# Kernel tuning notes

Measured on AMD Instinct MI355X. Metric: run time of the kernel, lower is better.

Reference implementation:

```python
import jax, jax.numpy as jnp
import numpy as np


def setup_inputs() -> dict:
    key = jax.random.key(0)
    ks = jax.random.split(key, 6)
    B, C, W, H = 8, 512, 64, 64
    return {
        "x": jax.random.normal(ks[0], (B, C, W, H), dtype=jnp.float32),
        "proj_query": jax.random.normal(ks[1], (C, W, H), dtype=jnp.float32),
        "key_w": jax.random.normal(ks[2], (C, C), dtype=jnp.float32) * 0.02,
        "key_b": jax.random.normal(ks[3], (C,), dtype=jnp.float32) * 0.02,
        "value_w": jax.random.normal(ks[4], (C, C), dtype=jnp.float32) * 0.02,
        "value_b": jax.random.normal(ks[5], (C,), dtype=jnp.float32) * 0.02,
        "gamma": jnp.ones((1,), dtype=jnp.float32),
    }


def reference(x, proj_query, key_w, key_b, value_w, value_b, gamma):
    B, C, W, H = x.shape
    N = W * H
    # fixed memory query: (C, N); torch builds B x N x C via permute
    q = proj_query.reshape(C, N)
    # 1x1 convs == per-pixel channel matmuls
    k = jnp.einsum('oc,bchw->bohw', key_w, x) + key_b[None, :, None, None]
    v = jnp.einsum('oc,bchw->bohw', value_w, x) + value_b[None, :, None, None]
    k = k.reshape(B, C, N)
    v = v.reshape(B, C, N)
    # energy = bmm(key [B,C,N], query^T [N,C]) -> B x C x C (channel attention)
    energy = jnp.einsum('bcn,dn->bcd', k, q)
    attention = jax.nn.softmax(energy, axis=-1)
    # out = bmm(attention^T [B,C,C], value [B,C,N]) -> B x C x N
    out = jnp.einsum('bdc,bdn->bcn', attention, v)
    out = out.reshape(B, C, W, H)
    return gamma * out + x
```

## Files before the change

kernel.cpp:

```cpp
#include <hip/hip_runtime.h>

typedef unsigned short u16;
typedef unsigned int u32;
typedef unsigned long long u64;
typedef _Float16 f16x8 __attribute__((ext_vector_type(8)));
typedef float f32x4 __attribute__((ext_vector_type(4)));

__device__ __forceinline__ u16 f2h(float f) {
  union { _Float16 h; u16 u; } c; c.h = (_Float16)f; return c.u;
}
__device__ __forceinline__ float h2f(u16 v) {
  union { u16 u; _Float16 h; } c; c.u = v; return (float)c.h;
}

__device__ __forceinline__ f32x4 mfma16(f16x8 a, f16x8 b, f32x4 c) {
  return __builtin_amdgcn_mfma_f32_16x16x32_f16(a, b, c, 0, 0, 0);
}

__device__ __forceinline__ void ld8f(const float* s, u16* o) {
  float4 a = *(const float4*)s;
  float4 b = *(const float4*)(s + 4);
  o[0] = f2h(a.x); o[1] = f2h(a.y); o[2] = f2h(a.z); o[3] = f2h(a.w);
  o[4] = f2h(b.x); o[5] = f2h(b.y); o[6] = f2h(b.z); o[7] = f2h(b.w);
}

__device__ __forceinline__ void glds16(const u16* g, u16* l) {
  __builtin_amdgcn_global_load_lds(
      reinterpret_cast<const __attribute__((address_space(1))) u32*>(reinterpret_cast<u64>(g)),
      reinterpret_cast<__attribute__((address_space(3))) u32*>(reinterpret_cast<u64>(l)),
      16, 0, 0);
}

template<int TM, int TN, bool NNB>
__device__ __forceinline__ void gemm_core(const u16* __restrict__ A, int lda,
                                          const u16* __restrict__ B, int ldb,
                                          int ksteps, u16* sA, u16* sB, f32x4 acc[TM][TN]) {
  const int t = threadIdx.x;
  const int lane = t & 63, wave = t >> 6;
  const int wm = wave >> 1, wn = wave & 1;
  const int m16 = lane & 15, q4 = lane >> 4;
  constexpr int BM = TM * 32, BN = TN * 32;
  constexpr int TILEA = BM * 32, TILEB = BN * 32;
  constexpr int APF = BM / 64;
  constexpr int BPF = BN / 64;

  int aoff[APF], asl[APF];
#pragma unroll
  for (int p = 0; p < APF; ++p) {
    int s = p * 256 + t, row = s >> 2;
    int kc = (s & 3) ^ ((row >> 1) & 3);
    aoff[p] = row * lda + kc * 8;
    asl[p] = (p * 256 + (t & 192)) * 8;
  }
  int boff[BPF], bsl[BPF];
  if constexpr (!NNB) {
#pragma unroll
    for (int p = 0; p < BPF; ++p) {
      int s = p * 256 + t, row = s >> 2;
      int kc = (s & 3) ^ ((row >> 1) & 3);
      boff[p] = row * ldb + kc * 8;
      bsl[p] = (p * 256 + (t & 192)) * 8;
    }
  }

  int aro[TM], bro[TN];
#pragma unroll
  for (int i = 0; i < TM; ++i) {
    int row = wm * TM * 16 + i * 16 + m16;
    aro[i] = row * 32 + ((q4 ^ ((row >> 1) & 3)) << 3);
  }
#pragma unroll
  for (int j = 0; j < TN; ++j) {
    int row = wn * TN * 16 + j * 16 + m16;
    bro[j] = row * 32 + ((q4 ^ ((row >> 1) & 3)) << 3);
  }

  const int bkk = (t >> 4) * 2;
  const int bnn = (t & 15) * 8;
  const int erot = t & 7;

#pragma unroll
  for (int p = 0; p < APF; ++p) glds16(A + aoff[p], sA + asl[p]);
  if constexpr (!NNB) {
#pragma unroll
    for (int p = 0; p < BPF; ++p) glds16(B + boff[p], sB + bsl[p]);
  } else {
    const u16* src = B + (size_t)bkk * ldb + bnn;
    int4 pb0 = *(const int4*)src;
    int4 pb1 = *(const int4*)(src + ldb);
    u16 a0[8], a1[8];
    *(int4*)a0 = pb0; *(int4*)a1 = pb1;
#pragma unroll
    for (int ee = 0; ee < 8; ++ee) {
      int e = (ee + erot) & 7;
      int n = bnn + e;
      int off = n * 32 + ((((bkk >> 3) ^ ((n >> 1) & 3))) << 3) + (bkk & 7);
      *(u32*)&sB[off] = (u32)a0[e] | ((u32)a1[e] << 16);
    }
  }
  __syncthreads();

  int4 nb0, nb1;
#pragma unroll 2
  for (int kt = 0; kt < ksteps; ++kt) {
    const int cur = kt & 1;
    const int nxt = cur ^ 1;
    const bool more = kt + 1 < ksteps;

    if (more) {
      const u16* An = A + (kt + 1) * 32;
#pragma unroll
      for (int p = 0; p < APF; ++p) glds16(An + aoff[p], sA + nxt * TILEA + asl[p]);
      if constexpr (!NNB) {
        const u16* Bn = B + (kt + 1) * 32;
#pragma unroll
        for (int p = 0; p < BPF; ++p) glds16(Bn + boff[p], sB + nxt * TILEB + bsl[p]);
      } else {
        const u16* src = B + ((size_t)(kt + 1) * 32 + bkk) * ldb + bnn;
        nb0 = *(const int4*)src;
        nb1 = *(const int4*)(src + ldb);
      }
    }

    const u16* dA = sA + cur * TILEA;
    const u16* dB = sB + cur * TILEB;
    f16x8 af[TM], bv[TN];
#pragma unroll
    for (int i = 0; i < TM; ++i) af[i] = *(const f16x8*)&dA[aro[i]];
#pragma unroll
    for (int j = 0; j < TN; ++j) bv[j] = *(const f16x8*)&dB[bro[j]];
#pragma unroll
    for (int i = 0; i < TM; ++i)
#pragma unroll
      for (int j = 0; j < TN; ++j)
        acc[i][j] = mfma16(af[i], bv[j], acc[i][j]);

    if constexpr (NNB) {
      if (more) {
        u16 a0[8], a1[8];
        *(int4*)a0 = nb0; *(int4*)a1 = nb1;
        u16* wB = sB + nxt * TILEB;
#pragma unroll
        for (int ee = 0; ee < 8; ++ee) {
          int e = (ee + erot) & 7;
          int n = bnn + e;
          int off = n * 32 + ((((bkk >> 3) ^ ((n >> 1) & 3))) << 3) + (bkk & 7);
          *(u32*)&wB[off] = (u32)a0[e] | ((u32)a1[e] << 16);
        }
      }
    }
    __syncthreads();
  }
}

__global__ __launch_bounds__(256) void cvt_x_kernel(const float* __restrict__ x, u16* __restrict__ xh) {
  size_t i = ((size_t)blockIdx.x * 256 + threadIdx.x) * 8;
  u16 o[8];
  ld8f(x + i, o);
  *(int4*)&xh[i] = *(int4*)o;
}

__global__ __launch_bounds__(256) void cvt_q_kernel(const float* __restrict__ q, u16* __restrict__ qh,
                                                    float* __restrict__ qs) {
  int row = blockIdx.x, t = threadIdx.x;
  float s = 0.f;
#pragma unroll
  for (int p = 0; p < 2; ++p) {
    size_t i = (size_t)row * 4096 + p * 2048 + t * 8;
    u16 o[8];
    ld8f(q + i, o);
#pragma unroll
    for (int e = 0; e < 8; ++e) s += h2f(o[e]);
    *(int4*)&qh[i] = *(int4*)o;
  }
  for (int off = 32; off; off >>= 1) s += __shfl_xor(s, off);
  __shared__ float wsum[4];
  if ((t & 63) == 0) wsum[t >> 6] = s;
  __syncthreads();
  if (t == 0) qs[row] = wsum[0] + wsum[1] + wsum[2] + wsum[3];
}

__global__ __launch_bounds__(256) void prep_kernel(const float* __restrict__ vw, u16* __restrict__ vwT,
                                                   const float* __restrict__ kw, u16* __restrict__ kwh,
                                                   float* __restrict__ beta) {
  int blk = blockIdx.x, t = threadIdx.x;
  if (blk < 256) {
    __shared__ u16 sT[32 * 33];
    int bx = blk & 15, by = blk >> 4;
#pragma unroll
    for (int p = 0; p < 4; ++p) {
      int idx = p * 256 + t; int r = idx >> 5, c = idx & 31;
      sT[r * 33 + c] = f2h(vw[(size_t)(by * 32 + r) * 512 + bx * 32 + c]);
    }
    __syncthreads();
#pragma unroll
    for (int p = 0; p < 4; ++p) {
      int idx = p * 256 + t; int r = idx >> 5, c = idx & 31;
      vwT[(size_t)(bx * 32 + r) * 512 + by * 32 + c] = sT[c * 33 + r];
    }
  } else if (blk < 384) {
    size_t i = ((size_t)(blk - 256) * 256 + t) * 8;
    u16 o[8];
    ld8f(kw + i, o);
    *(int4*)&kwh[i] = *(int4*)o;
  } else {
    for (int i = t; i < 4096; i += 256) beta[i] = 0.f;
  }
}

__global__ __launch_bounds__(256) void sgemm_kernel(const u16* __restrict__ qh, const u16* __restrict__ xh,
                                                    u16* __restrict__ Sh) {
  __shared__ __align__(16) u16 sA[2 * 64 * 32], sB[2 * 64 * 32];
  int rt = blockIdx.x, jt = blockIdx.y;
  f32x4 acc[2][2];
#pragma unroll
  for (int i = 0; i < 2; ++i)
#pragma unroll
    for (int j = 0; j < 2; ++j) acc[i][j] = (f32x4){0.f, 0.f, 0.f, 0.f};
  gemm_core<2, 2, false>(qh + (size_t)jt * 64 * 4096, 4096,
                         xh + (size_t)rt * 64 * 4096, 4096, 128, sA, sB, acc);

  const int t = threadIdx.x, lane = t & 63, wave = t >> 6;
  const int wm = wave >> 1, wn = wave & 1, m16 = lane & 15, q4 = lane >> 4;
  int b = (rt * 64) >> 9, o0 = (rt * 64) & 511;
  u16* Ob = Sh + (size_t)b * 262144;
#pragma unroll
  for (int i = 0; i < 2; ++i)
#pragma unroll
    for (int j = 0; j < 2; ++j)
#pragma unroll
      for (int r = 0; r < 4; ++r) {
        int y = jt * 64 + wm * 32 + i * 16 + q4 * 4 + r;
        int o = o0 + wn * 32 + j * 16 + m16;
        Ob[(size_t)y * 512 + o] = f2h(acc[i][j][r]);
      }
}

__global__ __launch_bounds__(256) void egemm_kernel(const u16* __restrict__ kwh, const u16* __restrict__ Sh,
                                                    float* __restrict__ E) {
  __shared__ __align__(16) u16 sA[2 * 64 * 32], sB[2 * 64 * 32];
  int xt = blockIdx.x >> 3, yt = blockIdx.x & 7, b = blockIdx.y;
  f32x4 acc[2][2];
#pragma unroll
  for (int i = 0; i < 2; ++i)
#pragma unroll
    for (int j = 0; j < 2; ++j) acc[i][j] = (f32x4){0.f, 0.f, 0.f, 0.f};
  gemm_core<2, 2, false>(kwh + (size_t)xt * 64 * 512, 512,
                         Sh + (size_t)b * 262144 + (size_t)yt * 64 * 512, 512, 16, sA, sB, acc);

  const int t = threadIdx.x, lane = t & 63, wave = t >> 6;
  const int wm = wave >> 1, wn = wave & 1, m16 = lane & 15, q4 = lane >> 4;
  float* O = E + ((size_t)b * 512 + xt * 64) * 512 + yt * 64;
#pragma unroll
  for (int i = 0; i < 2; ++i)
#pragma unroll
    for (int j = 0; j < 2; ++j)
#pragma unroll
      for (int r = 0; r < 4; ++r) {
        int row = wm * 32 + i * 16 + q4 * 4 + r;
        int col = wn * 32 + j * 16 + m16;
        O[(size_t)row * 512 + col] = acc[i][j][r];
      }
}

__global__ __launch_bounds__(256) void softmax_kernel(const float* __restrict__ E, const float* __restrict__ qs,
                                                      const float* __restrict__ kb, const float* __restrict__ vb,
                                                      u16* __restrict__ attT, float* __restrict__ beta) {
  __shared__ float sE[16 * 516];
  __shared__ float sM[16], sS[16];
  int i0 = blockIdx.x * 16, b = blockIdx.y, t = threadIdx.x;
  const float* Eb = E + ((size_t)b * 512 + i0) * 512;
  for (int ch = 0; ch < 32; ++ch) {
    int idx = ch * 256 + t;
    int row = idx >> 9, col = idx & 511;
    sE[row * 516 + col] = Eb[(size_t)row * 512 + col] + kb[i0 + row] * qs[col];
  }
  __syncthreads();
  {
    int row = t >> 4, sub = t & 15;
    float mx = -1e30f;
    for (int ii = 0; ii < 32; ++ii) mx = fmaxf(mx, sE[row * 516 + sub + ii * 16]);
    for (int off = 8; off; off >>= 1) mx = fmaxf(mx, __shfl_xor(mx, off));
    float sm = 0.f;
    for (int ii = 0; ii < 32; ++ii) sm += __expf(sE[row * 516 + sub + ii * 16] - mx);
    for (int off = 8; off; off >>= 1) sm += __shfl_xor(sm, off);
    if (sub == 0) { sM[row] = mx; sS[row] = 1.f / sm; }
  }
  __syncthreads();
  float vbr = vb[i0 + (t & 15)];
  u16* Ob = attT + (size_t)b * 262144;
  for (int ch = 0; ch < 32; ++ch) {
    int idx = ch * 256 + t;
    int r = idx & 15, j = idx >> 4;
    float a = __expf(sE[r * 516 + j] - sM[r]) * sS[r];
    Ob[(size_t)j * 512 + i0 + r] = f2h(a);
    float part = a * vbr;
    for (int off = 8; off; off >>= 1) part += __shfl_xor(part, off);
    if (r == 0) atomicAdd(&beta[b * 512 + j], part);
  }
}

__global__ __launch_bounds__(256) void wgemm_kernel(const u16* __restrict__ attT, const u16* __restrict__ vwT,
                                                    u16* __restrict__ W) {
  __shared__ __align__(16) u16 sA[2 * 64 * 32], sB[2 * 64 * 32];
  int ct = blockIdx.x >> 3, ot = blockIdx.x & 7, b = blockIdx.y;
  f32x4 acc[2][2];
#pragma unroll
  for (int i = 0; i < 2; ++i)
#pragma unroll
    for (int j = 0; j < 2; ++j) acc[i][j] = (f32x4){0.f, 0.f, 0.f, 0.f};
  gemm_core<2, 2, false>(attT + (size_t)b * 262144 + (size_t)ct * 64 * 512, 512,
                         vwT + (size_t)ot * 64 * 512, 512, 16, sA, sB, acc);

  const int t = threadIdx.x, lane = t & 63, wave = t >> 6;
  const int wm = wave >> 1, wn = wave & 1, m16 = lane & 15, q4 = lane >> 4;
  u16* O = W + (size_t)b * 262144 + (size_t)(ct * 64) * 512 + ot * 64;
#pragma unroll
  for (int i = 0; i < 2; ++i)
#pragma unroll
    for (int j = 0; j < 2; ++j)
#pragma unroll
      for (int r = 0; r < 4; ++r) {
        int row = wm * 32 + i * 16 + q4 * 4 + r;
        int col = wn * 32 + j * 16 + m16;
        O[(size_t)row * 512 + col] = f2h(acc[i][j][r]);
      }
}

__global__ __launch_bounds__(256) void outgemm_kernel(const u16* __restrict__ W, const u16* __restrict__ xh,
                                                      const float* __restrict__ x, const float* __restrict__ beta,
                                                      const float* __restrict__ gm, float* __restrict__ out) {
  __shared__ __align__(16) u16 sA[2 * 128 * 32], sB[2 * 128 * 32];
  int nt = blockIdx.x, ct = blockIdx.y, b = blockIdx.z;
  f32x4 acc[4][4];
#pragma unroll
  for (int i = 0; i < 4; ++i)
#pragma unroll
    for (int j = 0; j < 4; ++j) acc[i][j] = (f32x4){0.f, 0.f, 0.f, 0.f};
  gemm_core<4, 4, true>(W + (size_t)b * 262144 + (size_t)ct * 128 * 512, 512,
                        xh + (size_t)b * 2097152 + nt * 128, 4096, 16, sA, sB, acc);

  const int t = threadIdx.x, lane = t & 63, wave = t >> 6;
  const int wm = wave >> 1, wn = wave & 1, m16 = lane & 15, q4 = lane >> 4;
  float g = gm[0];
#pragma unroll
  for (int i = 0; i < 4; ++i)
#pragma unroll
    for (int j = 0; j < 4; ++j)
#pragma unroll
      for (int r = 0; r < 4; ++r) {
        int c = ct * 128 + wm * 64 + i * 16 + q4 * 4 + r;
        int n = nt * 128 + wn * 64 + j * 16 + m16;
        size_t idx = (size_t)b * 2097152 + (size_t)c * 4096 + n;
        out[idx] = g * (acc[i][j][r] + beta[b * 512 + c]) + x[idx];
      }
}

extern "C" void kernel_launch(void* const* d_in, const int* in_sizes, int n_in,
                              void* d_out, int out_size, void* d_ws, size_t ws_size,
                              hipStream_t stream) {
  const float* x  = (const float*)d_in[0];
  const float* pq = (const float*)d_in[1];
  const float* kw = (const float*)d_in[2];
  const float* kb = (const float*)d_in[3];
  const float* vw = (const float*)d_in[4];
  const float* vb = (const float*)d_in[5];
  const float* gm = (const float*)d_in[6];
  float* out = (float*)d_out;

  char* ws = (char*)d_ws;
  u16*   xh   = (u16*)(ws);
  u16*   qh   = (u16*)(ws + (32ull << 20));
  u16*   Sh   = (u16*)(ws + (36ull << 20));
  u16*   W    = (u16*)(ws + (36ull << 20));
  float* E    = (float*)(ws + (40ull << 20));
  u16*   attT = (u16*)(ws + (48ull << 20));
  u16*   kwh  = (u16*)(ws + (52ull << 20));
  u16*   vwT  = (u16*)(ws + (52ull << 20) + 524288);
  char*  sm   = ws + (53ull << 20);
  float* qs   = (float*)(sm);
  float* beta = (float*)(sm + 4096);

  cvt_x_kernel<<<dim3(8192), 256, 0, stream>>>(x, xh);
  cvt_q_kernel<<<dim3(512), 256, 0, stream>>>(pq, qh, qs);
  prep_kernel<<<dim3(385), 256, 0, stream>>>(vw, vwT, kw, kwh, beta);
  sgemm_kernel<<<dim3(64, 8), 256, 0, stream>>>(qh, xh, Sh);
  egemm_kernel<<<dim3(64, 8), 256, 0, stream>>>(kwh, Sh, E);
  softmax_kernel<<<dim3(32, 8), 256, 0, stream>>>(E, qs, kb, vb, attT, beta);
  wgemm_kernel<<<dim3(64, 8), 256, 0, stream>>>(attT, vwT, W);
  outgemm_kernel<<<dim3(32, 4, 8), 256, 0, stream>>>(W, xh, x, beta, gm, out);
}
```

Baseline: 245.8 us.

## Triple-buffer GEMM LDS tiles with one barrier per k-step and explicit waitcnts

Reworks the shared gemm_core pipeline from double-buffered LDS with two __syncthreads per iteration to a rotating triple buffer (A, and B when loaded via global_load_lds). Each step uses a single s_barrier preceded by hand-placed s_waitcnt on outstanding vector-memory loads, so the next tile's async loads can stay in flight across the barrier. The transposed B writes in the NNB path use precomputed offsets with a parity swizzle in place of a rotation. All GEMM kernels get larger LDS allocations, which may lower occupancy, and the hand-written waitcnt counts must exactly match the issued loads to stay correct.

```diff
diff --git a/kernel.cpp b/kernel.cpp
--- a/kernel.cpp
+++ b/kernel.cpp
@@ -43,6 +43,7 @@
   constexpr int TILEA = BM * 32, TILEB = BN * 32;
   constexpr int APF = BM / 64;
   constexpr int BPF = BN / 64;
+  constexpr int VPI = NNB ? (APF + 2) : (APF + BPF);
 
   int aoff[APF], asl[APF];
 #pragma unroll
@@ -77,58 +78,78 @@
 
   const int bkk = (t >> 4) * 2;
   const int bnn = (t & 15) * 8;
-  const int erot = t & 7;
-
-#pragma unroll
-  for (int p = 0; p < APF; ++p) glds16(A + aoff[p], sA + asl[p]);
+  const int bpar = (t >> 2) & 1;
+  int bwo[8];
+  if constexpr (NNB) {
+#pragma unroll
+    for (int ee = 0; ee < 8; ++ee) {
+      int n = bnn + (ee ^ bpar);
+      bwo[ee] = n * 32 + (((bkk >> 3) ^ ((n >> 1) & 3)) << 3) + (bkk & 7);
+    }
+  }
+
+  u16 *aR = sA, *aS = sA + TILEA, *aT = sA + 2 * TILEA;
+  u16 *bR = sB, *bS = sB + TILEB, *bT = sB + 2 * TILEB;
+
+  int4 nb0, nb1;
+  if constexpr (NNB) {
+    const u16* src = B + (size_t)bkk * ldb + bnn;
+    nb0 = *(const int4*)src;
+    nb1 = *(const int4*)(src + ldb);
+    __builtin_amdgcn_sched_barrier(0);
+  }
+#pragma unroll
+  for (int p = 0; p < APF; ++p) glds16(A + aoff[p], aR + asl[p]);
   if constexpr (!NNB) {
 #pragma unroll
-    for (int p = 0; p < BPF; ++p) glds16(B + boff[p], sB + bsl[p]);
+    for (int p = 0; p < BPF; ++p) glds16(B + boff[p], bR + bsl[p]);
   } else {
-    const u16* src = B + (size_t)bkk * ldb + bnn;
-    int4 pb0 = *(const int4*)src;
-    int4 pb1 = *(const int4*)(src + ldb);
-    u16 a0[8], a1[8];
-    *(int4*)a0 = pb0; *(int4*)a1 = pb1;
-#pragma unroll
-    for (int ee = 0; ee < 8; ++ee) {
-      int e = (ee + erot) & 7;
-      int n = bnn + e;
-      int off = n * 32 + ((((bkk >> 3) ^ ((n >> 1) & 3))) << 3) + (bkk & 7);
-      *(u32*)&sB[off] = (u32)a0[e] | ((u32)a1[e] << 16);
-    }
-  }
-  __syncthreads();
-
-  int4 nb0, nb1;
-#pragma unroll 2
+    union { int4 v; u16 h[8]; } u0, u1; u0.v = nb0; u1.v = nb1;
+    u32 val[8];
+#pragma unroll
+    for (int e = 0; e < 8; ++e) val[e] = (u32)u0.h[e] | ((u32)u1.h[e] << 16);
+#pragma unroll
+    for (int ee = 0; ee < 8; ++ee)
+      *(u32*)&bR[bwo[ee]] = bpar ? val[ee ^ 1] : val[ee];
+  }
+
+#pragma unroll 1
   for (int kt = 0; kt < ksteps; ++kt) {
-    const int cur = kt & 1;
-    const int nxt = cur ^ 1;
     const bool more = kt + 1 < ksteps;
 
     if (more) {
-      const u16* An = A + (kt + 1) * 32;
-#pragma unroll
-      for (int p = 0; p < APF; ++p) glds16(An + aoff[p], sA + nxt * TILEA + asl[p]);
-      if constexpr (!NNB) {
-        const u16* Bn = B + (kt + 1) * 32;
-#pragma unroll
-        for (int p = 0; p < BPF; ++p) glds16(Bn + boff[p], sB + nxt * TILEB + bsl[p]);
-      } else {
+      if constexpr (NNB) {
         const u16* src = B + ((size_t)(kt + 1) * 32 + bkk) * ldb + bnn;
         nb0 = *(const int4*)src;
         nb1 = *(const int4*)(src + ldb);
-      }
-    }
-
-    const u16* dA = sA + cur * TILEA;
-    const u16* dB = sB + cur * TILEB;
+        __builtin_amdgcn_sched_barrier(0);
+      }
+      const u16* An = A + (kt + 1) * 32;
+#pragma unroll
+      for (int p = 0; p < APF; ++p) glds16(An + aoff[p], aS + asl[p]);
+      if constexpr (!NNB) {
+        const u16* Bn = B + (kt + 1) * 32;
+#pragma unroll
+        for (int p = 0; p < BPF; ++p) glds16(Bn + boff[p], bS + bsl[p]);
+      }
+      if constexpr (NNB)
+        asm volatile("s_waitcnt vmcnt(%0) lgkmcnt(0)" :: "n"(VPI) : "memory");
+      else
+        asm volatile("s_waitcnt vmcnt(%0)" :: "n"(VPI) : "memory");
+    } else {
+      if constexpr (NNB)
+        asm volatile("s_waitcnt vmcnt(0) lgkmcnt(0)" ::: "memory");
+      else
+        asm volatile("s_waitcnt vmcnt(0)" ::: "memory");
+    }
+    __builtin_amdgcn_s_barrier();
+    __builtin_amdgcn_sched_barrier(0);
+
     f16x8 af[TM], bv[TN];
 #pragma unroll
-    for (int i = 0; i < TM; ++i) af[i] = *(const f16x8*)&dA[aro[i]];
-#pragma unroll
-    for (int j = 0; j < TN; ++j) bv[j] = *(const f16x8*)&dB[bro[j]];
+    for (int i = 0; i < TM; ++i) af[i] = *(const f16x8*)&aR[aro[i]];
+#pragma unroll
+    for (int j = 0; j < TN; ++j) bv[j] = *(const f16x8*)&bR[bro[j]];
 #pragma unroll
     for (int i = 0; i < TM; ++i)
 #pragma unroll
@@ -137,19 +158,19 @@
 
     if constexpr (NNB) {
       if (more) {
-        u16 a0[8], a1[8];
-        *(int4*)a0 = nb0; *(int4*)a1 = nb1;
-        u16* wB = sB + nxt * TILEB;
-#pragma unroll
-        for (int ee = 0; ee < 8; ++ee) {
-          int e = (ee + erot) & 7;
-          int n = bnn + e;
-          int off = n * 32 + ((((bkk >> 3) ^ ((n >> 1) & 3))) << 3) + (bkk & 7);
-          *(u32*)&wB[off] = (u32)a0[e] | ((u32)a1[e] << 16);
-        }
-      }
-    }
-    __syncthreads();
+        union { int4 v; u16 h[8]; } u0, u1; u0.v = nb0; u1.v = nb1;
+        u32 val[8];
+#pragma unroll
+        for (int e = 0; e < 8; ++e) val[e] = (u32)u0.h[e] | ((u32)u1.h[e] << 16);
+#pragma unroll
+        for (int ee = 0; ee < 8; ++ee)
+          *(u32*)&bS[bwo[ee]] = bpar ? val[ee ^ 1] : val[ee];
+      }
+    }
+
+    { u16* x = aR; aR = aS; aS = aT; aT = x; }
+    if constexpr (!NNB) { u16* x = bR; bR = bS; bS = bT; bT = x; }
+    else               { u16* x = bR; bR = bS; bS = x; }
   }
 }
 
@@ -210,7 +231,7 @@
 
 __global__ __launch_bounds__(256) void sgemm_kernel(const u16* __restrict__ qh, const u16* __restrict__ xh,
                                                     u16* __restrict__ Sh) {
-  __shared__ __align__(16) u16 sA[2 * 64 * 32], sB[2 * 64 * 32];
+  __shared__ __align__(16) u16 sA[3 * 64 * 32], sB[3 * 64 * 32];
   int rt = blockIdx.x, jt = blockIdx.y;
   f32x4 acc[2][2];
 #pragma unroll
@@ -238,7 +259,7 @@
 
 __global__ __launch_bounds__(256) void egemm_kernel(const u16* __restrict__ kwh, const u16* __restrict__ Sh,
                                                     float* __restrict__ E) {
-  __shared__ __align__(16) u16 sA[2 * 64 * 32], sB[2 * 64 * 32];
+  __shared__ __align__(16) u16 sA[3 * 64 * 32], sB[3 * 64 * 32];
   int xt = blockIdx.x >> 3, yt = blockIdx.x & 7, b = blockIdx.y;
   f32x4 acc[2][2];
 #pragma unroll
@@ -302,7 +323,7 @@
 
 __global__ __launch_bounds__(256) void wgemm_kernel(const u16* __restrict__ attT, const u16* __restrict__ vwT,
                                                     u16* __restrict__ W) {
-  __shared__ __align__(16) u16 sA[2 * 64 * 32], sB[2 * 64 * 32];
+  __shared__ __align__(16) u16 sA[3 * 64 * 32], sB[3 * 64 * 32];
   int ct = blockIdx.x >> 3, ot = blockIdx.x & 7, b = blockIdx.y;
   f32x4 acc[2][2];
 #pragma unroll
@@ -330,7 +351,7 @@
 __global__ __launch_bounds__(256) void outgemm_kernel(const u16* __restrict__ W, const u16* __restrict__ xh,
                                                       const float* __restrict__ x, const float* __restrict__ beta,
                                                       const float* __restrict__ gm, float* __restrict__ out) {
-  __shared__ __align__(16) u16 sA[2 * 128 * 32], sB[2 * 128 * 32];
+  __shared__ __align__(16) u16 sA[3 * 128 * 32], sB[2 * 128 * 32];
   int nt = blockIdx.x, ct = blockIdx.y, b = blockIdx.z;
   f32x4 acc[4][4];
 #pragma unroll
```

Result: faster. 238.6 us (-2.9%).
